# Performance work log

Hardware: AMD Instinct MI355X
Metric: run time of the kernel (lower is better)

## Reference

```python
import jax, jax.numpy as jnp
import numpy as np


def setup_inputs() -> dict:
    key = jax.random.key(0)
    k1, k2 = jax.random.split(key)
    bs, seq_len, n_sources, input_dim = 16, 4096, 4, 257
    predictions = jax.random.normal(k1, (bs, seq_len, n_sources, input_dim), dtype=jnp.float32)
    ground_truths = jax.random.normal(k2, (bs, seq_len, n_sources, input_dim), dtype=jnp.float32)
    return {"predictions": predictions, "ground_truths": ground_truths}


def reference(predictions, ground_truths):
    # metric == 'euclidean' branch: dist[b, s] = ||pred[b,:,s,:] - gt[b,:,s,:]||_2
    diff = predictions - ground_truths                      # [bs, seq, src, dim]
    dists = jnp.sqrt(jnp.sum(diff * diff, axis=(1, 3)))     # [bs, src]
    return jnp.sum(dists)                                   # scalar loss
```

## Files before the change

### kernel.cpp

```cpp
#include <hip/hip_runtime.h>
#include <math.h>

#define BS   16
#define SEQ  4096
#define SRC  4
#define DIM  257
#define NBUCKET (BS * SRC)
#define CHUNKS 32
#define ROWS_PER_BLOCK (SEQ / CHUNKS)

__global__ __launch_bounds__(256) void bucket_sq_sums(
    const float* __restrict__ pred,
    const float* __restrict__ gt,
    float* __restrict__ ws)
{
    const int bucket = blockIdx.x;
    const int b      = bucket >> 2;
    const int src    = bucket & 3;
    const int chunk  = blockIdx.y;
    const int wave   = threadIdx.x >> 6;
    const int lane   = threadIdx.x & 63;

    const int k0    = (4 - src) & 3;
    const int n4    = (DIM - k0) >> 2;
    const int nscal = DIM - (n4 << 2);

    float acc = 0.0f;

    for (int r = wave; r < ROWS_PER_BLOCK; r += 4) {
        const int s_seq = chunk * ROWS_PER_BLOCK + r;
        const long long base =
            ((long long)(b * SEQ + s_seq) * SRC + src) * (long long)DIM;

        if (lane < n4) {
            const float4* p4 = (const float4*)(pred + base + k0);
            const float4* g4 = (const float4*)(gt   + base + k0);
            float4 p = p4[lane];
            float4 g = g4[lane];
            float dx = p.x - g.x;
            float dy = p.y - g.y;
            float dz = p.z - g.z;
            float dw = p.w - g.w;
            acc += dx * dx + dy * dy + dz * dz + dw * dw;
        }
        if (lane < nscal) {
            const int off = (lane < k0) ? lane : (k0 + (n4 << 2) + (lane - k0));
            const float d = pred[base + off] - gt[base + off];
            acc += d * d;
        }
    }

    #pragma unroll
    for (int o = 32; o > 0; o >>= 1) acc += __shfl_down(acc, o, 64);

    __shared__ float s[4];
    if (lane == 0) s[wave] = acc;
    __syncthreads();
    if (threadIdx.x == 0) {
        atomicAdd(&ws[bucket], s[0] + s[1] + s[2] + s[3]);
    }
}

__global__ void finalize_kernel(const float* __restrict__ ws,
                                float* __restrict__ out)
{
    const int t = threadIdx.x;
    float v = sqrtf(ws[t]);
    #pragma unroll
    for (int o = 32; o > 0; o >>= 1) v += __shfl_down(v, o, 64);
    if (t == 0) out[0] = v;
}

extern "C" void kernel_launch(void* const* d_in, const int* in_sizes, int n_in,
                              void* d_out, int out_size, void* d_ws, size_t ws_size,
                              hipStream_t stream)
{
    const float* pred = (const float*)d_in[0];
    const float* gt   = (const float*)d_in[1];
    float* ws  = (float*)d_ws;
    float* out = (float*)d_out;

    hipMemsetAsync(ws, 0, NBUCKET * sizeof(float), stream);

    bucket_sq_sums<<<dim3(NBUCKET, CHUNKS), 256, 0, stream>>>(pred, gt, ws);
    finalize_kernel<<<1, 64, 0, stream>>>(ws, out);
}
```

Measured before the change: 509.2 us.

## Process full seq rows with aligned float4 loads and fuse finalize via last-block

Each block now handles a whole row of 4 sources (1028 floats, 257 float4s) so every thread issues aligned float4 loads, and it attributes squared differences to sources with per-thread weight masks instead of using per-source scalar tails. The chunk count rises and the grid changes to batch by chunk. The separate finalize kernel is replaced by a last-block-done pattern using an atomic counter and a threadfence, which removes one kernel launch. This adds four-way shuffle reductions and one extra atomic per block.

```diff
diff --git a/kernel.cpp b/kernel.cpp
--- a/kernel.cpp
+++ b/kernel.cpp
@@ -5,70 +5,102 @@
 #define SEQ  4096
 #define SRC  4
 #define DIM  257
+#define ROW4 257
 #define NBUCKET (BS * SRC)
-#define CHUNKS 32
-#define ROWS_PER_BLOCK (SEQ / CHUNKS)
+#define CHUNKS 128
+#define RPB (SEQ / CHUNKS)
+#define NBLOCKS (BS * CHUNKS)
 
-__global__ __launch_bounds__(256) void bucket_sq_sums(
+__device__ __forceinline__ int src_of(int e) {
+    return (e >= DIM) + (e >= 2 * DIM) + (e >= 3 * DIM);
+}
+
+__global__ __launch_bounds__(256) void fused_dist_kernel(
     const float* __restrict__ pred,
     const float* __restrict__ gt,
-    float* __restrict__ ws)
+    float* __restrict__ ws,
+    float* __restrict__ out)
 {
-    const int bucket = blockIdx.x;
-    const int b      = bucket >> 2;
-    const int src    = bucket & 3;
-    const int chunk  = blockIdx.y;
-    const int wave   = threadIdx.x >> 6;
-    const int lane   = threadIdx.x & 63;
+    const int b     = blockIdx.x;
+    const int chunk = blockIdx.y;
+    const int t     = threadIdx.x;
+    const int lane  = t & 63;
+    const int wave  = t >> 6;
 
-    const int k0    = (4 - src) & 3;
-    const int n4    = (DIM - k0) >> 2;
-    const int nscal = DIM - (n4 << 2);
+    const int   e0  = t << 2;
+    const int   sLo = src_of(e0);
+    const float wh1 = (float)(src_of(e0 + 1) != sLo);
+    const float wh2 = (float)(src_of(e0 + 2) != sLo);
+    const float wh3 = (float)(src_of(e0 + 3) != sLo);
+    const int   sHi = (sLo < 3) ? sLo + 1 : 3;
 
-    float acc = 0.0f;
+    const float4* __restrict__ P = (const float4*)pred;
+    const float4* __restrict__ G = (const float4*)gt;
+    const int row4_base = (b * SEQ + chunk * RPB) * ROW4;
 
-    for (int r = wave; r < ROWS_PER_BLOCK; r += 4) {
-        const int s_seq = chunk * ROWS_PER_BLOCK + r;
-        const long long base =
-            ((long long)(b * SEQ + s_seq) * SRC + src) * (long long)DIM;
+    float accAll = 0.0f;
+    float accHi  = 0.0f;
+    float accT   = 0.0f;
 
-        if (lane < n4) {
-            const float4* p4 = (const float4*)(pred + base + k0);
-            const float4* g4 = (const float4*)(gt   + base + k0);
-            float4 p = p4[lane];
-            float4 g = g4[lane];
-            float dx = p.x - g.x;
-            float dy = p.y - g.y;
-            float dz = p.z - g.z;
-            float dw = p.w - g.w;
-            acc += dx * dx + dy * dy + dz * dz + dw * dw;
-        }
-        if (lane < nscal) {
-            const int off = (lane < k0) ? lane : (k0 + (n4 << 2) + (lane - k0));
-            const float d = pred[base + off] - gt[base + off];
-            acc += d * d;
-        }
+    #pragma unroll 2
+    for (int r = 0; r < RPB; ++r) {
+        const int i = row4_base + r * ROW4 + t;
+        float4 p = P[i];
+        float4 g = G[i];
+        float dx = p.x - g.x, dy = p.y - g.y, dz = p.z - g.z, dw = p.w - g.w;
+        float d2x = dx * dx, d2y = dy * dy, d2z = dz * dz, d2w = dw * dw;
+        accAll += (d2x + d2y) + (d2z + d2w);
+        accHi = fmaf(d2y, wh1, accHi);
+        accHi = fmaf(d2z, wh2, accHi);
+        accHi = fmaf(d2w, wh3, accHi);
     }
 
+    for (int r = t; r < RPB; r += 256) {
+        const int i = row4_base + r * ROW4 + 256;
+        float4 p = P[i];
+        float4 g = G[i];
+        float dx = p.x - g.x, dy = p.y - g.y, dz = p.z - g.z, dw = p.w - g.w;
+        accT += (dx * dx + dy * dy) + (dz * dz + dw * dw);
+    }
+
+    const float accLo = accAll - accHi;
+    float a0 = (sLo == 0 ? accLo : 0.0f) + (sHi == 0 ? accHi : 0.0f);
+    float a1 = (sLo == 1 ? accLo : 0.0f) + (sHi == 1 ? accHi : 0.0f);
+    float a2 = (sLo == 2 ? accLo : 0.0f) + (sHi == 2 ? accHi : 0.0f);
+    float a3 = (sLo == 3 ? accLo : 0.0f) + (sHi == 3 ? accHi : 0.0f) + accT;
+
     #pragma unroll
-    for (int o = 32; o > 0; o >>= 1) acc += __shfl_down(acc, o, 64);
+    for (int o = 32; o > 0; o >>= 1) {
+        a0 += __shfl_down(a0, o, 64);
+        a1 += __shfl_down(a1, o, 64);
+        a2 += __shfl_down(a2, o, 64);
+        a3 += __shfl_down(a3, o, 64);
+    }
 
-    __shared__ float s[4];
-    if (lane == 0) s[wave] = acc;
+    __shared__ float sred[4][4];
+    __shared__ int isLast;
+    if (lane == 0) {
+        sred[wave][0] = a0; sred[wave][1] = a1;
+        sred[wave][2] = a2; sred[wave][3] = a3;
+    }
     __syncthreads();
-    if (threadIdx.x == 0) {
-        atomicAdd(&ws[bucket], s[0] + s[1] + s[2] + s[3]);
+    if (t < 4) {
+        atomicAdd(&ws[b * SRC + t],
+                  sred[0][t] + sred[1][t] + sred[2][t] + sred[3][t]);
     }
-}
-
-__global__ void finalize_kernel(const float* __restrict__ ws,
-                                float* __restrict__ out)
-{
-    const int t = threadIdx.x;
-    float v = sqrtf(ws[t]);
-    #pragma unroll
-    for (int o = 32; o > 0; o >>= 1) v += __shfl_down(v, o, 64);
-    if (t == 0) out[0] = v;
+    __threadfence();
+    __syncthreads();
+    if (t == 0) {
+        unsigned prev = atomicAdd((unsigned*)(ws + NBUCKET), 1u);
+        isLast = (prev == (unsigned)(NBLOCKS - 1));
+    }
+    __syncthreads();
+    if (isLast && wave == 0) {
+        float v = sqrtf(atomicAdd(&ws[lane], 0.0f));
+        #pragma unroll
+        for (int o = 32; o > 0; o >>= 1) v += __shfl_down(v, o, 64);
+        if (lane == 0) out[0] = v;
+    }
 }
 
 extern "C" void kernel_launch(void* const* d_in, const int* in_sizes, int n_in,
@@ -80,8 +112,7 @@
     float* ws  = (float*)d_ws;
     float* out = (float*)d_out;
 
-    hipMemsetAsync(ws, 0, NBUCKET * sizeof(float), stream);
+    hipMemsetAsync(ws, 0, (NBUCKET + 1) * sizeof(float), stream);
 
-    bucket_sq_sums<<<dim3(NBUCKET, CHUNKS), 256, 0, stream>>>(pred, gt, ws);
-    finalize_kernel<<<1, 64, 0, stream>>>(ws, out);
+    fused_dist_kernel<<<dim3(BS, CHUNKS), 256, 0, stream>>>(pred, gt, ws, out);
 }
```

After: 864.5 us. 1.7x slower.
